# Kernel tuning notes

Hardware: AMD Instinct MI355X
Metric: run time of the kernel (lower is better)

Reference implementation:

```python
import jax, jax.numpy as jnp
import numpy as np

LR = 0.01
WD = 0.01


def _lfltm(params, x):
    w1, b1, w2, b2 = params
    return jnp.tanh(x @ w1 + b1) @ w2 + b2  # [N, D]


def _deep_opt_elem(Wm1, bm1, Wm2, bm2, g):
    # per-parameter-element learned optimizer: scalar grad -> hidden(M) -> scalar update
    h = jnp.tanh(g[..., None] * Wm1 + bm1)  # [..., M]
    return h @ Wm2 + bm2[0]


def setup_inputs() -> dict:
    key = jax.random.key(0)
    ks = jax.random.split(key, 8)
    N, D, H, M = 16384, 512, 1024, 32
    return {
        "x_t": jax.random.normal(ks[0], (N, D), jnp.float32),
        "x_target": jax.random.normal(ks[1], (N, D), jnp.float32),
        "w1": jax.random.normal(ks[2], (D, H), jnp.float32) * 0.02,
        "b1": jnp.zeros((H,), jnp.float32),
        "w2": jax.random.normal(ks[3], (H, D), jnp.float32) * 0.02,
        "b2": jnp.zeros((D,), jnp.float32),
        "Wm1": jax.random.normal(ks[4], (M,), jnp.float32) * 0.1,
        "bm1": jnp.zeros((M,), jnp.float32),
        "Wm2": jax.random.normal(ks[5], (M,), jnp.float32) * 0.1,
        "bm2": jnp.zeros((1,), jnp.float32),
    }


def reference(x_t, x_target, w1, b1, w2, b2, Wm1, bm1, Wm2, bm2):
    mem = (w1, b1, w2, b2)

    # retrieve: h_t = LFLTM(memory_state, x_t)
    h_t = _lfltm(mem, x_t)

    # analytic per-step gradient of MSE loss through the memory MLP
    def compute_loss(params):
        pred = _lfltm(params, x_t)
        return jnp.mean((pred - x_target) ** 2)

    grads = jax.grad(compute_loss)(mem)

    # learned optimizer on each gradient tensor, then fast-weight update
    new_mem = tuple(
        p - (LR * _deep_opt_elem(Wm1, bm1, Wm2, bm2, g) + WD * p)
        for p, g in zip(mem, grads)
    )

    return (h_t,) + new_mem
```

## Files before the change

### kernel.cpp

```cpp
#include <hip/hip_runtime.h>
#include <hip/hip_bf16.h>

#define LR 0.01f
#define WD 0.01f
#define NTHREADS 256
#define SCALE_G 1048576.0f
#define INV_SCALE_G 9.5367431640625e-07f
#define TRS 136

typedef short s16x8 __attribute__((ext_vector_type(8)));
typedef _Float16 f16x8 __attribute__((ext_vector_type(8)));
typedef float f32x4 __attribute__((ext_vector_type(4)));
typedef unsigned short u16;

__device__ __forceinline__ u16 f2h(float f) {
    _Float16 h = (_Float16)f;
    return *reinterpret_cast<u16*>(&h);
}
__device__ __forceinline__ float h2f(u16 u) {
    _Float16 h;
    *reinterpret_cast<u16*>(&h) = u;
    return (float)h;
}
__device__ __forceinline__ float tanh_fast(float x) {
    float t = fminf(fmaxf(2.f * x, -30.f), 30.f);
    float e = __expf(t);
    return 1.f - 2.f * __builtin_amdgcn_rcpf(e + 1.f);
}

__device__ __forceinline__ void stage_pair(const u16* gA, const u16* gB, int ldg,
                                           u16* lds) {
    const int t = threadIdx.x;
#pragma unroll
    for (int q = 0; q < 4; ++q) {
        int s = t + q * 256;
        int row = s >> 3, chp = s & 7;
        int chl = chp ^ (row & 7);
        const u16* gp = (chl < 4) ? (gA + (size_t)row * ldg + chl * 8)
                                  : (gB + (size_t)row * ldg + (chl & 3) * 8);
        __builtin_amdgcn_global_load_lds(
            (const __attribute__((address_space(1))) void*)gp,
            (__attribute__((address_space(3))) void*)(lds + s * 8), 16, 0, 0);
    }
}

__device__ __forceinline__ f16x8 frag(const u16* P, int r, int c) {
    return *(const f16x8*)(P + r * 64 + ((c ^ (r & 7)) * 8));
}

template <int EPI>
__global__ __launch_bounds__(NTHREADS) void k_mfma(
    const u16* __restrict__ A, const u16* __restrict__ Bt,
    int nbx, int Md, int Nd, int Kd, int Kslice,
    const float* __restrict__ bias, const float* __restrict__ xtgt,
    const u16* __restrict__ Th,
    float* __restrict__ outf, u16* __restrict__ outb, u16* __restrict__ outbT,
    float* __restrict__ gbias, float scale) {
    __shared__ u16 smem[128 * TRS];
    __shared__ float colacc[128];

    const int nwg = gridDim.x;
    const int sw = (blockIdx.x & 7) * (nwg >> 3) + (blockIdx.x >> 3);
    const int m0 = (sw / nbx) * 128, n0 = (sw % nbx) * 128;
    const int kb = blockIdx.y * Kslice;

    const int lane = threadIdx.x & 63, wid = threadIdx.x >> 6;
    const int wrow = (wid >> 1) * 64, wcol = (wid & 1) * 64;
    const int lm = lane & 15;
    const int cA = lane >> 4;

    f32x4 acc[4][4] = {};

    const u16* gA = A + (size_t)m0 * Kd + kb;
    const u16* gB = Bt + (size_t)n0 * Kd + kb;

    if (EPI == 1 || EPI == 2)
        if (threadIdx.x < 128) colacc[threadIdx.x] = 0.f;

    stage_pair(gA, gB, Kd, smem);
    __syncthreads();

    int cur = 0;
    for (int k0 = 0; k0 < Kslice; k0 += 32, cur ^= 1) {
        if (k0 + 32 < Kslice)
            stage_pair(gA + k0 + 32, gB + k0 + 32, Kd, smem + (cur ^ 1) * 8192);
        const u16* P1 = smem + cur * 8192;
        f16x8 a[4], b[4];
#pragma unroll
        for (int i = 0; i < 4; ++i) {
            a[i] = frag(P1, wrow + i * 16 + lm, cA);
            b[i] = frag(P1, wcol + i * 16 + lm, cA + 4);
        }
#pragma unroll
        for (int i = 0; i < 4; ++i)
#pragma unroll
            for (int j = 0; j < 4; ++j)
                acc[i][j] = __builtin_amdgcn_mfma_f32_16x16x32_f16(
                    a[i], b[j], acc[i][j], 0, 0, 0);
        __syncthreads();
    }

    const int rbase = (lane >> 4) * 4;

    if (EPI == 3) {
#pragma unroll
        for (int i = 0; i < 4; ++i) {
            const int row0 = m0 + wrow + i * 16 + rbase;
#pragma unroll
            for (int j = 0; j < 4; ++j) {
                const int col = n0 + wcol + j * 16 + lm;
#pragma unroll
                for (int r = 0; r < 4; ++r)
                    atomicAdd(&outf[(size_t)(row0 + r) * Nd + col], acc[i][j][r]);
            }
        }
        return;
    }

    ushort4 hv[4][4];
#pragma unroll
    for (int i = 0; i < 4; ++i) {
        const int row0 = m0 + wrow + i * 16 + rbase;
#pragma unroll
        for (int j = 0; j < 4; ++j) {
            const int col = n0 + wcol + j * 16 + lm;
            if (EPI == 0) {
                float bcol = bias[col];
                hv[i][j].x = f2h(tanh_fast(acc[i][j][0] + bcol));
                hv[i][j].y = f2h(tanh_fast(acc[i][j][1] + bcol));
                hv[i][j].z = f2h(tanh_fast(acc[i][j][2] + bcol));
                hv[i][j].w = f2h(tanh_fast(acc[i][j][3] + bcol));
            } else if (EPI == 1) {
                float csum = 0.f;
                float bcol = bias[col];
#pragma unroll
                for (int r = 0; r < 4; ++r) {
                    size_t idx = (size_t)(row0 + r) * Nd + col;
                    float p = acc[i][j][r] + bcol;
                    outf[idx] = p;
                    float gf = scale * (p - xtgt[idx]);
                    csum += gf;
                    ((u16*)&hv[i][j])[r] = f2h(gf);
                }
                atomicAdd(&colacc[wcol + j * 16 + lm], csum);
            } else {
                float csum = 0.f;
#pragma unroll
                for (int r = 0; r < 4; ++r) {
                    size_t idx = (size_t)(row0 + r) * Nd + col;
                    float tv = h2f(Th[idx]);
                    float da = acc[i][j][r] * (1.0f - tv * tv);
                    csum += da;
                    ((u16*)&hv[i][j])[r] = f2h(da);
                }
                atomicAdd(&colacc[wcol + j * 16 + lm], csum);
            }
        }
    }

#pragma unroll
    for (int i = 0; i < 4; ++i)
#pragma unroll
        for (int j = 0; j < 4; ++j)
            *(ushort4*)(smem + (wcol + j * 16 + lm) * TRS + (wrow + i * 16 + rbase)) =
                hv[i][j];
    __syncthreads();
#pragma unroll
    for (int p = 0; p < 8; ++p) {
        int tr = wid * 32 + p * 4 + (lane >> 4);
        int ch = lane & 15;
        s16x8 v = *(const s16x8*)(smem + tr * TRS + ch * 8);
        *(s16x8*)(outbT + (size_t)(n0 + tr) * Md + m0 + ch * 8) = v;
    }

    if (EPI <= 1) {
        __syncthreads();
#pragma unroll
        for (int i = 0; i < 4; ++i)
#pragma unroll
            for (int j = 0; j < 4; ++j)
#pragma unroll
                for (int r = 0; r < 4; ++r)
                    smem[(wrow + i * 16 + rbase + r) * TRS + wcol + j * 16 + lm] =
                        ((u16*)&hv[i][j])[r];
        __syncthreads();
#pragma unroll
        for (int p = 0; p < 8; ++p) {
            int rr = wid * 32 + p * 4 + (lane >> 4);
            int ch = lane & 15;
            s16x8 v = *(const s16x8*)(smem + rr * TRS + ch * 8);
            *(s16x8*)(outb + (size_t)(m0 + rr) * Nd + n0 + ch * 8) = v;
        }
    }

    if (EPI == 1 || EPI == 2) {
        __syncthreads();
        if (threadIdx.x < 128)
            atomicAdd(&gbias[n0 + threadIdx.x], colacc[threadIdx.x]);
    }
}

__global__ void k_prep(const float* __restrict__ in, u16* __restrict__ rm,
                       u16* __restrict__ tr, int R, int C) {
    __shared__ float tile[64][65];
    const int tx = threadIdx.x & 63, ty = threadIdx.x >> 6;
    const int c0 = blockIdx.x * 64, r0 = blockIdx.y * 64;
#pragma unroll
    for (int i = 0; i < 64; i += 4) {
        size_t idx = (size_t)(r0 + ty + i) * C + c0 + tx;
        float v = in[idx];
        tile[ty + i][tx] = v;
        if (rm) rm[idx] = f2h(v);
    }
    __syncthreads();
    if (tr) {
#pragma unroll
        for (int i = 0; i < 64; i += 4)
            tr[(size_t)(c0 + ty + i) * R + r0 + tx] = f2h(tile[tx][ty + i]);
    }
}

__global__ void k_update_all(
    const float* __restrict__ w1, const float* __restrict__ b1,
    const float* __restrict__ w2, const float* __restrict__ b2,
    const float* __restrict__ g, float* __restrict__ out,
    int n1, int n2, int n3, int n4,
    const float* __restrict__ Wm1, const float* __restrict__ bm1,
    const float* __restrict__ Wm2, const float* __restrict__ bm2,
    int M, float invScale) {
    __shared__ float s1[64], s2[64], s3[64];
    if (threadIdx.x < M) {
        s1[threadIdx.x] = Wm1[threadIdx.x];
        s2[threadIdx.x] = bm1[threadIdx.x];
        s3[threadIdx.x] = Wm2[threadIdx.x];
    }
    __syncthreads();
    int i = blockIdx.x * blockDim.x + threadIdx.x;
    int n = n1 + n2 + n3 + n4;
    if (i >= n) return;
    const float* p;
    int off;
    if (i < n1) { p = w1; off = 0; }
    else if (i < n1 + n2) { p = b1; off = n1; }
    else if (i < n1 + n2 + n3) { p = w2; off = n1 + n2; }
    else { p = b2; off = n1 + n2 + n3; }
    float gv = g[i] * invScale;
    float u = bm2[0];
#pragma unroll 8
    for (int m = 0; m < M; ++m) u += tanh_fast(fmaf(gv, s1[m], s2[m])) * s3[m];
    float pv = p[i - off];
    out[i] = pv - (LR * u + WD * pv);
}

__global__ void k_zero(float* __restrict__ p, int n) {
    int i = blockIdx.x * blockDim.x + threadIdx.x;
    if (i < n) p[i] = 0.f;
}

extern "C" void kernel_launch(void* const* d_in, const int* in_sizes, int n_in,
                              void* d_out, int out_size, void* d_ws, size_t ws_size,
                              hipStream_t stream) {
    const float* x_t      = (const float*)d_in[0];
    const float* x_target = (const float*)d_in[1];
    const float* w1  = (const float*)d_in[2];
    const float* b1  = (const float*)d_in[3];
    const float* w2  = (const float*)d_in[4];
    const float* b2  = (const float*)d_in[5];
    const float* Wm1 = (const float*)d_in[6];
    const float* bm1 = (const float*)d_in[7];
    const float* Wm2 = (const float*)d_in[8];
    const float* bm2 = (const float*)d_in[9];

    const int H = in_sizes[3];
    const int D = in_sizes[5];
    const int N = in_sizes[0] / D;
    const int M = in_sizes[6];

    char* w = (char*)d_ws;
    float* gw1 = (float*)w;            w += (size_t)D * H * 4;
    float* gb1 = (float*)w;            w += (size_t)H * 4;
    float* gw2 = (float*)w;            w += (size_t)H * D * 4;
    float* gb2 = (float*)w;            w += (size_t)D * 4;
    u16* Tf   = (u16*)w;               w += (size_t)N * H * 2;
    u16* TT   = (u16*)w;               w += (size_t)N * H * 2;
    u16* dAT  = (u16*)w;               w += (size_t)N * H * 2;
    u16* Gb   = (u16*)w;               w += (size_t)N * D * 2;
    u16* GT   = (u16*)w;               w += (size_t)N * D * 2;
    u16* xf   = (u16*)w;               w += (size_t)N * D * 2;
    u16* xT   = (u16*)w;               w += (size_t)N * D * 2;
    u16* w1T  = (u16*)w;               w += (size_t)D * H * 2;
    u16* w2T  = (u16*)w;               w += (size_t)D * H * 2;
    u16* w2b  = (u16*)w;               w += (size_t)H * D * 2;

    float* out  = (float*)d_out;
    float* h_t  = out;
    float* o_w1 = h_t + (size_t)N * D;

    dim3 blk(NTHREADS);
    const float scaleG = (2.0f / ((float)N * (float)D)) * SCALE_G;

    int zn = D * H + H + H * D + D;
    k_zero<<<dim3((zn + NTHREADS - 1) / NTHREADS), blk, 0, stream>>>(gw1, zn);

    k_prep<<<dim3(D / 64, N / 64), blk, 0, stream>>>(x_t, xf, xT, N, D);
    k_prep<<<dim3(H / 64, D / 64), blk, 0, stream>>>(w1, nullptr, w1T, D, H);
    k_prep<<<dim3(D / 64, H / 64), blk, 0, stream>>>(w2, w2b, w2T, H, D);

    k_mfma<0><<<dim3((H / 128) * (N / 128), 1), blk, 0, stream>>>(
        xf, w1T, H / 128, N, H, D, D, b1, nullptr, nullptr,
        nullptr, Tf, TT, nullptr, 0.f);

    k_mfma<1><<<dim3((D / 128) * (N / 128), 1), blk, 0, stream>>>(
        Tf, w2T, D / 128, N, D, H, H, b2, x_target, nullptr,
        h_t, Gb, GT, gb2, scaleG);

    k_mfma<2><<<dim3((H / 128) * (N / 128), 1), blk, 0, stream>>>(
        Gb, w2b, H / 128, N, H, D, D, nullptr, nullptr, Tf,
        nullptr, nullptr, dAT, gb1, 0.f);

    const int SPLIT = 16;
    k_mfma<3><<<dim3((D / 128) * (H / 128), SPLIT), blk, 0, stream>>>(
        TT, GT, D / 128, H, D, N, N / SPLIT, nullptr, nullptr, nullptr,
        gw2, nullptr, nullptr, nullptr, 0.f);

    k_mfma<3><<<dim3((H / 128) * (D / 128), SPLIT), blk, 0, stream>>>(
        xT, dAT, H / 128, D, H, N, N / SPLIT, nullptr, nullptr, nullptr,
        gw1, nullptr, nullptr, nullptr, 0.f);

    int nAll = D * H + H + H * D + D;
    k_update_all<<<dim3((nAll + NTHREADS - 1) / NTHREADS), blk, 0, stream>>>(
        w1, b1, w2, b2, gw1, o_w1, D * H, H, H * D, D,
        Wm1, bm1, Wm2, bm2, M, INV_SCALE_G);
}
```

Measured before the change: 380.8 us.

## Enlarge GEMM tiles to 256x128 with 512 threads and triple-buffered K pipeline

After: 385.4 us. Within noise of the previous version (+1.2%).

```diff
diff --git a/kernel.cpp b/kernel.cpp
--- a/kernel.cpp
+++ b/kernel.cpp
@@ -3,10 +3,12 @@
 
 #define LR 0.01f
 #define WD 0.01f
-#define NTHREADS 256
 #define SCALE_G 1048576.0f
 #define INV_SCALE_G 9.5367431640625e-07f
-#define TRS 136
+
+#define BUFU 24576
+#define TRT 264
+#define RMS 136
 
 typedef short s16x8 __attribute__((ext_vector_type(8)));
 typedef _Float16 f16x8 __attribute__((ext_vector_type(8)));
@@ -28,86 +30,124 @@
     return 1.f - 2.f * __builtin_amdgcn_rcpf(e + 1.f);
 }
 
-__device__ __forceinline__ void stage_pair(const u16* gA, const u16* gB, int ldg,
-                                           u16* lds) {
-    const int t = threadIdx.x;
-#pragma unroll
-    for (int q = 0; q < 4; ++q) {
-        int s = t + q * 256;
-        int row = s >> 3, chp = s & 7;
-        int chl = chp ^ (row & 7);
-        const u16* gp = (chl < 4) ? (gA + (size_t)row * ldg + chl * 8)
-                                  : (gB + (size_t)row * ldg + (chl & 3) * 8);
-        __builtin_amdgcn_global_load_lds(
-            (const __attribute__((address_space(1))) void*)gp,
-            (__attribute__((address_space(3))) void*)(lds + s * 8), 16, 0, 0);
-    }
-}
-
-__device__ __forceinline__ f16x8 frag(const u16* P, int r, int c) {
-    return *(const f16x8*)(P + r * 64 + ((c ^ (r & 7)) * 8));
-}
+__device__ __forceinline__ void stage_A(const u16* gA, int ldg, u16* lds, int q) {
+    int s = threadIdx.x + q * 512;
+    int row = s >> 3, chp = s & 7;
+    int chl = chp ^ (row & 7);
+    __builtin_amdgcn_global_load_lds(
+        (const __attribute__((address_space(1))) void*)(gA + (size_t)row * ldg + chl * 8),
+        (__attribute__((address_space(3))) void*)(lds + s * 8), 16, 0, 0);
+}
+__device__ __forceinline__ void stage_B(const u16* gB, int ldg, u16* lds, int q) {
+    int s = threadIdx.x + q * 512;
+    int row = s >> 3, chp = s & 7;
+    int chl = chp ^ (row & 7);
+    __builtin_amdgcn_global_load_lds(
+        (const __attribute__((address_space(1))) void*)(gB + (size_t)row * ldg + chl * 8),
+        (__attribute__((address_space(3))) void*)(lds + 16384 + s * 8), 16, 0, 0);
+}
+
+__device__ __forceinline__ f16x8 fragA(const u16* P, int r, int ks, int hi) {
+    return *(const f16x8*)(P + r * 64 + ((((ks << 2) | hi)) ^ (r & 7)) * 8);
+}
+__device__ __forceinline__ f16x8 fragB(const u16* P, int r, int ks, int hi) {
+    return *(const f16x8*)(P + 16384 + r * 64 + ((((ks << 2) | hi)) ^ (r & 7)) * 8);
+}
+
+#define MEMFENCE asm volatile("" ::: "memory")
 
 template <int EPI>
-__global__ __launch_bounds__(NTHREADS) void k_mfma(
+__global__ __launch_bounds__(512) void k_mfma(
     const u16* __restrict__ A, const u16* __restrict__ Bt,
     int nbx, int Md, int Nd, int Kd, int Kslice,
     const float* __restrict__ bias, const float* __restrict__ xtgt,
     const u16* __restrict__ Th,
     float* __restrict__ outf, u16* __restrict__ outb, u16* __restrict__ outbT,
     float* __restrict__ gbias, float scale) {
-    __shared__ u16 smem[128 * TRS];
+    __shared__ u16 smem[3 * BUFU];
     __shared__ float colacc[128];
 
     const int nwg = gridDim.x;
     const int sw = (blockIdx.x & 7) * (nwg >> 3) + (blockIdx.x >> 3);
-    const int m0 = (sw / nbx) * 128, n0 = (sw % nbx) * 128;
+    const int m0 = (sw / nbx) * 256, n0 = (sw % nbx) * 128;
     const int kb = blockIdx.y * Kslice;
 
     const int lane = threadIdx.x & 63, wid = threadIdx.x >> 6;
-    const int wrow = (wid >> 1) * 64, wcol = (wid & 1) * 64;
+    const int wrow = (wid >> 2) * 128;
+    const int wcol = (wid & 3) * 32;
     const int lm = lane & 15;
-    const int cA = lane >> 4;
-
-    f32x4 acc[4][4] = {};
+    const int hi = lane >> 4;
+
+    f32x4 acc[8][2] = {};
 
     const u16* gA = A + (size_t)m0 * Kd + kb;
     const u16* gB = Bt + (size_t)n0 * Kd + kb;
+    const int nt = Kslice >> 6;
 
     if (EPI == 1 || EPI == 2)
         if (threadIdx.x < 128) colacc[threadIdx.x] = 0.f;
 
-    stage_pair(gA, gB, Kd, smem);
-    __syncthreads();
-
-    int cur = 0;
-    for (int k0 = 0; k0 < Kslice; k0 += 32, cur ^= 1) {
-        if (k0 + 32 < Kslice)
-            stage_pair(gA + k0 + 32, gB + k0 + 32, Kd, smem + (cur ^ 1) * 8192);
-        const u16* P1 = smem + cur * 8192;
-        f16x8 a[4], b[4];
-#pragma unroll
-        for (int i = 0; i < 4; ++i) {
-            a[i] = frag(P1, wrow + i * 16 + lm, cA);
-            b[i] = frag(P1, wcol + i * 16 + lm, cA + 4);
+    for (int q = 0; q < 4; ++q) stage_A(gA, Kd, smem, q);
+    for (int q = 0; q < 2; ++q) stage_B(gB, Kd, smem, q);
+    for (int q = 0; q < 4; ++q) stage_A(gA + 64, Kd, smem + BUFU, q);
+    for (int q = 0; q < 2; ++q) stage_B(gB + 64, Kd, smem + BUFU, q);
+    asm volatile("s_waitcnt vmcnt(6)" ::: "memory");
+    MEMFENCE; __builtin_amdgcn_s_barrier(); MEMFENCE;
+
+    for (int t = 0; t < nt; ++t) {
+        u16* P = smem + (t % 3) * BUFU;
+        u16* Pn = smem + ((t + 2) % 3) * BUFU;
+        const u16* gA2 = gA + (size_t)(t + 2) * 64;
+        const u16* gB2 = gB + (size_t)(t + 2) * 64;
+        const bool st = (t + 2) < nt;
+        f16x8 bfr[2][2];
+#pragma unroll
+        for (int p = 0; p < 4; ++p) {
+            f16x8 afr[2][2];
+#pragma unroll
+            for (int mm = 0; mm < 2; ++mm)
+#pragma unroll
+                for (int ks = 0; ks < 2; ++ks)
+                    afr[mm][ks] = fragA(P, wrow + (2 * p + mm) * 16 + lm, ks, hi);
+            if (p == 0) {
+#pragma unroll
+                for (int j = 0; j < 2; ++j)
+#pragma unroll
+                    for (int ks = 0; ks < 2; ++ks)
+                        bfr[j][ks] = fragB(P, wcol + j * 16 + lm, ks, hi);
+            }
+            if (st) {
+                if (p == 0) { stage_A(gA2, Kd, Pn, 0); stage_A(gA2, Kd, Pn, 1); }
+                else if (p == 1) { stage_A(gA2, Kd, Pn, 2); stage_A(gA2, Kd, Pn, 3); }
+                else if (p == 2) { stage_B(gB2, Kd, Pn, 0); stage_B(gB2, Kd, Pn, 1); }
+            }
+            MEMFENCE; __builtin_amdgcn_s_barrier(); MEMFENCE;
+            __builtin_amdgcn_s_setprio(1);
+#pragma unroll
+            for (int mm = 0; mm < 2; ++mm)
+#pragma unroll
+                for (int j = 0; j < 2; ++j)
+#pragma unroll
+                    for (int ks = 0; ks < 2; ++ks)
+                        acc[2 * p + mm][j] = __builtin_amdgcn_mfma_f32_16x16x32_f16(
+                            afr[mm][ks], bfr[j][ks], acc[2 * p + mm][j], 0, 0, 0);
+            __builtin_amdgcn_s_setprio(0);
+            if (p == 3) {
+                if (t + 2 < nt)      asm volatile("s_waitcnt vmcnt(6)" ::: "memory");
+                else if (t + 1 < nt) asm volatile("s_waitcnt vmcnt(0)" ::: "memory");
+            }
+            MEMFENCE; __builtin_amdgcn_s_barrier(); MEMFENCE;
         }
-#pragma unroll
-        for (int i = 0; i < 4; ++i)
-#pragma unroll
-            for (int j = 0; j < 4; ++j)
-                acc[i][j] = __builtin_amdgcn_mfma_f32_16x16x32_f16(
-                    a[i], b[j], acc[i][j], 0, 0, 0);
-        __syncthreads();
-    }
-
-    const int rbase = (lane >> 4) * 4;
+    }
+
+    const int rbase = hi * 4;
 
     if (EPI == 3) {
 #pragma unroll
-        for (int i = 0; i < 4; ++i) {
+        for (int i = 0; i < 8; ++i) {
             const int row0 = m0 + wrow + i * 16 + rbase;
 #pragma unroll
-            for (int j = 0; j < 4; ++j) {
+            for (int j = 0; j < 2; ++j) {
                 const int col = n0 + wcol + j * 16 + lm;
 #pragma unroll
                 for (int r = 0; r < 4; ++r)
@@ -117,12 +157,12 @@
         return;
     }
 
-    ushort4 hv[4][4];
-#pragma unroll
-    for (int i = 0; i < 4; ++i) {
+    ushort4 hv[8][2];
+#pragma unroll
+    for (int i = 0; i < 8; ++i) {
         const int row0 = m0 + wrow + i * 16 + rbase;
 #pragma unroll
-        for (int j = 0; j < 4; ++j) {
+        for (int j = 0; j < 2; ++j) {
             const int col = n0 + wcol + j * 16 + lm;
             if (EPI == 0) {
                 float bcol = bias[col];
@@ -131,14 +171,13 @@
                 hv[i][j].z = f2h(tanh_fast(acc[i][j][2] + bcol));
                 hv[i][j].w = f2h(tanh_fast(acc[i][j][3] + bcol));
             } else if (EPI == 1) {
-                float csum = 0.f;
-                float bcol = bias[col];
+                float csum = 0.f, bcol = bias[col];
 #pragma unroll
                 for (int r = 0; r < 4; ++r) {
                     size_t idx = (size_t)(row0 + r) * Nd + col;
-                    float p = acc[i][j][r] + bcol;
-                    outf[idx] = p;
-                    float gf = scale * (p - xtgt[idx]);
+                    float pv = acc[i][j][r] + bcol;
+                    outf[idx] = pv;
+                    float gf = scale * (pv - xtgt[idx]);
                     csum += gf;
                     ((u16*)&hv[i][j])[r] = f2h(gf);
                 }
@@ -158,37 +197,38 @@
         }
     }
 
-#pragma unroll
-    for (int i = 0; i < 4; ++i)
-#pragma unroll
-        for (int j = 0; j < 4; ++j)
-            *(ushort4*)(smem + (wcol + j * 16 + lm) * TRS + (wrow + i * 16 + rbase)) =
+    __syncthreads();
+#pragma unroll
+    for (int i = 0; i < 8; ++i)
+#pragma unroll
+        for (int j = 0; j < 2; ++j)
+            *(ushort4*)(smem + (wcol + j * 16 + lm) * TRT + wrow + i * 16 + rbase) =
                 hv[i][j];
     __syncthreads();
 #pragma unroll
     for (int p = 0; p < 8; ++p) {
-        int tr = wid * 32 + p * 4 + (lane >> 4);
-        int ch = lane & 15;
-        s16x8 v = *(const s16x8*)(smem + tr * TRS + ch * 8);
-        *(s16x8*)(outbT + (size_t)(n0 + tr) * Md + m0 + ch * 8) = v;
+        int cid = threadIdx.x + p * 512;
+        int trr = cid >> 5, ch = cid & 31;
+        s16x8 v = *(const s16x8*)(smem + trr * TRT + ch * 8);
+        *(s16x8*)(outbT + (size_t)(n0 + trr) * Md + m0 + ch * 8) = v;
     }
 
     if (EPI <= 1) {
         __syncthreads();
 #pragma unroll
-        for (int i = 0; i < 4; ++i)
-#pragma unroll
-            for (int j = 0; j < 4; ++j)
+        for (int i = 0; i < 8; ++i)
+#pragma unroll
+            for (int j = 0; j < 2; ++j)
 #pragma unroll
                 for (int r = 0; r < 4; ++r)
-                    smem[(wrow + i * 16 + rbase + r) * TRS + wcol + j * 16 + lm] =
+                    smem[(wrow + i * 16 + rbase + r) * RMS + wcol + j * 16 + lm] =
                         ((u16*)&hv[i][j])[r];
         __syncthreads();
 #pragma unroll
         for (int p = 0; p < 8; ++p) {
-            int rr = wid * 32 + p * 4 + (lane >> 4);
-            int ch = lane & 15;
-            s16x8 v = *(const s16x8*)(smem + rr * TRS + ch * 8);
+            int cid = threadIdx.x + p * 512;
+            int rr = cid >> 4, ch = cid & 15;
+            s16x8 v = *(const s16x8*)(smem + rr * RMS + ch * 8);
             *(s16x8*)(outb + (size_t)(m0 + rr) * Nd + n0 + ch * 8) = v;
         }
     }
@@ -296,39 +336,39 @@
     float* h_t  = out;
     float* o_w1 = h_t + (size_t)N * D;
 
-    dim3 blk(NTHREADS);
+    dim3 blk(256), blkG(512);
     const float scaleG = (2.0f / ((float)N * (float)D)) * SCALE_G;
 
     int zn = D * H + H + H * D + D;
-    k_zero<<<dim3((zn + NTHREADS - 1) / NTHREADS), blk, 0, stream>>>(gw1, zn);
+    k_zero<<<dim3((zn + 255) / 256), blk, 0, stream>>>(gw1, zn);
 
     k_prep<<<dim3(D / 64, N / 64), blk, 0, stream>>>(x_t, xf, xT, N, D);
     k_prep<<<dim3(H / 64, D / 64), blk, 0, stream>>>(w1, nullptr, w1T, D, H);
     k_prep<<<dim3(D / 64, H / 64), blk, 0, stream>>>(w2, w2b, w2T, H, D);
 
-    k_mfma<0><<<dim3((H / 128) * (N / 128), 1), blk, 0, stream>>>(
+    k_mfma<0><<<dim3((N / 256) * (H / 128), 1), blkG, 0, stream>>>(
         xf, w1T, H / 128, N, H, D, D, b1, nullptr, nullptr,
         nullptr, Tf, TT, nullptr, 0.f);
 
-    k_mfma<1><<<dim3((D / 128) * (N / 128), 1), blk, 0, stream>>>(
+    k_mfma<1><<<dim3((N / 256) * (D / 128), 1), blkG, 0, stream>>>(
         Tf, w2T, D / 128, N, D, H, H, b2, x_target, nullptr,
         h_t, Gb, GT, gb2, scaleG);
 
-    k_mfma<2><<<dim3((H / 128) * (N / 128), 1), blk, 0, stream>>>(
+    k_mfma<2><<<dim3((N / 256) * (H / 128), 1), blkG, 0, stream>>>(
         Gb, w2b, H / 128, N, H, D, D, nullptr, nullptr, Tf,
         nullptr, nullptr, dAT, gb1, 0.f);
 
     const int SPLIT = 16;
-    k_mfma<3><<<dim3((D / 128) * (H / 128), SPLIT), blk, 0, stream>>>(
+    k_mfma<3><<<dim3((H / 256) * (D / 128), SPLIT), blkG, 0, stream>>>(
         TT, GT, D / 128, H, D, N, N / SPLIT, nullptr, nullptr, nullptr,
         gw2, nullptr, nullptr, nullptr, 0.f);
 
-    k_mfma<3><<<dim3((H / 128) * (D / 128), SPLIT), blk, 0, stream>>>(
+    k_mfma<3><<<dim3((D / 256) * (H / 128), SPLIT), blkG, 0, stream>>>(
         xT, dAT, H / 128, D, H, N, N / SPLIT, nullptr, nullptr, nullptr,
         gw1, nullptr, nullptr, nullptr, 0.f);
 
     int nAll = D * H + H + H * D + D;
-    k_update_all<<<dim3((nAll + NTHREADS - 1) / NTHREADS), blk, 0, stream>>>(
+    k_update_all<<<dim3((nAll + 255) / 256), blk, 0, stream>>>(
         w1, b1, w2, b2, gw1, o_w1, D * H, H, H * D, D,
         Wm1, bm1, Wm2, bm2, M, INV_SCALE_G);
 }
```
